# Kernel tuning notes

Hardware: AMD Instinct MI355X
Metric: run time of the kernel (lower is better)

The kernel has to match this reference:

```python
import jax, jax.numpy as jnp
import numpy as np

MAX_NORM = 1.0 - 1e-5  # Poincare ball (c=1) boundary clip, geoopt-style
NUM_HEADS = 8

def _norm(x):
    return jnp.sqrt(jnp.sum(x * x, axis=-1, keepdims=True) + 1e-30)

def projx(x):
    n = _norm(x)
    return jnp.where(n > MAX_NORM, x * (MAX_NORM / n), x)

def expmap0(u):
    n = _norm(u)
    return jnp.tanh(n) * u / n

def logmap0(x):
    n = _norm(x)
    return jnp.arctanh(jnp.minimum(n, MAX_NORM)) * x / n

def mobius_add(x, y):
    xy = jnp.sum(x * y, axis=-1, keepdims=True)
    x2 = jnp.sum(x * x, axis=-1, keepdims=True)
    y2 = jnp.sum(y * y, axis=-1, keepdims=True)
    num = (1.0 + 2.0 * xy + y2) * x + (1.0 - x2) * y
    den = 1.0 + 2.0 * xy + x2 * y2
    return num / jnp.maximum(den, 1e-15)

def mobius_matvec(M, x):
    xn = _norm(x)
    mx = x @ M.T
    mxn = _norm(mx)
    return jnp.tanh(mxn / xn * jnp.arctanh(jnp.minimum(xn, MAX_NORM))) * mx / mxn

def man_linear(x, W, b):
    # Manifold_Linear: mobius matvec + mobius bias add + project (geoopt MobiusLinear)
    return projx(mobius_add(mobius_matvec(W, x), b))

def mob_relu(x):
    # Mob_Act(ReLU): act in tangent space at origin
    return projx(expmap0(jax.nn.relu(logmap0(x))))

def layer_norm(x, g, b):
    mu = jnp.mean(x, axis=-1, keepdims=True)
    v = jnp.var(x, axis=-1, keepdims=True)
    return (x - mu) / jnp.sqrt(v + 1e-5) * g + b

def mha_tan_space(x_q, x_kv, Wq, bq, Wk, bk, Wv, bv, Wo, bo, num_heads):
    # ManifoldMHA with att_metric='tan_space': manifold linear projections,
    # scaled dot-product attention in the tangent space at the origin.
    q = logmap0(man_linear(x_q, Wq, bq))   # (S, B, E)
    k = logmap0(man_linear(x_kv, Wk, bk))  # (T, B, E)
    v = logmap0(man_linear(x_kv, Wv, bv))  # (T, B, E)
    S, B, E = q.shape
    hd = E // num_heads
    def split(t):  # (T,B,E) -> (B,H,T,hd)
        return t.reshape(t.shape[0], B, num_heads, hd).transpose(1, 2, 0, 3)
    qh, kh, vh = split(q), split(k), split(v)
    scores = jnp.einsum('bhqd,bhkd->bhqk', qh, kh) / np.sqrt(hd).astype(np.float32)
    attn = jax.nn.softmax(scores, axis=-1)
    o = jnp.einsum('bhqk,bhkd->bhqd', attn, vh)  # (B,H,S,hd)
    o = o.transpose(2, 0, 1, 3).reshape(S, B, E)
    o = expmap0(o)
    return man_linear(o, Wo, bo)

def forward_block(x, ln1_g, ln1_b, ln2_g, ln2_b, Wq, bq, Wk, bk, Wv, bv, Wo, bo, W1, b1, W2, b2):
    residual = x
    h = expmap0(layer_norm(logmap0(x), ln1_g, ln1_b))
    h = mha_tan_space(h, h, Wq, bq, Wk, bk, Wv, bv, Wo, bo, NUM_HEADS)
    h = projx(h)
    h = projx(mobius_add(h, residual))
    residual = h
    h = projx(expmap0(layer_norm(logmap0(h), ln2_g, ln2_b)))
    h = mob_relu(man_linear(h, W1, b1))   # fc1 = Manifold_Linear + Mob_Act
    h = projx(h)                          # act_dropout (identity, eval) + projx
    h = mob_relu(man_linear(h, W2, b2))   # fc2
    h = projx(mobius_add(h, residual))
    return h

def setup_inputs() -> dict:
    key = jax.random.key(0)
    ks = jax.random.split(key, 18)
    S, B, E, F = 128, 256, 512, 2048
    sE = 1.0 / np.sqrt(E)
    sF = 1.0 / np.sqrt(F)
    # input points must lie inside the unit ball: randn scaled small
    x = jax.random.normal(ks[0], (S, B, E), jnp.float32) * 0.02
    def w(k, o, i, s):
        return jax.random.normal(k, (o, i), jnp.float32) * s
    def bias(k, d):
        return jax.random.normal(k, (d,), jnp.float32) * 1e-3
    return {
        'x': x,
        'ln1_g': jnp.ones((E,), jnp.float32), 'ln1_b': jnp.zeros((E,), jnp.float32),
        'ln2_g': jnp.ones((E,), jnp.float32), 'ln2_b': jnp.zeros((E,), jnp.float32),
        'Wq': w(ks[1], E, E, sE), 'bq': bias(ks[2], E),
        'Wk': w(ks[3], E, E, sE), 'bk': bias(ks[4], E),
        'Wv': w(ks[5], E, E, sE), 'bv': bias(ks[6], E),
        'Wo': w(ks[7], E, E, sE), 'bo': bias(ks[8], E),
        'W1': w(ks[9], F, E, sE), 'b1': bias(ks[10], F),
        'W2': w(ks[11], E, F, sF), 'b2': bias(ks[12], E),
    }

def reference(x, ln1_g, ln1_b, ln2_g, ln2_b, Wq, bq, Wk, bk, Wv, bv, Wo, bo, W1, b1, W2, b2):
    return forward_block(x, ln1_g, ln1_b, ln2_g, ln2_b, Wq, bq, Wk, bk, Wv, bv, Wo, bo, W1, b1, W2, b2)
```

## Files before the change

kernel.cpp:

```cpp
#include <hip/hip_runtime.h>
#include <math.h>

#define S_DIM 128
#define B_DIM 256
#define E_DIM 512
#define F_DIM 2048
#define N_ROWS (S_DIM * B_DIM)
#define CH 8192
#define MAXN 0.99999f

typedef __bf16 bf16x8 __attribute__((ext_vector_type(8)));
typedef float f32x4 __attribute__((ext_vector_type(4)));

__device__ __forceinline__ float frcp(float x) { return __builtin_amdgcn_rcpf(x); }
__device__ __forceinline__ float frsq(float x) { return __builtin_amdgcn_rsqf(x); }
__device__ __forceinline__ float fexp2(float x) { return __builtin_amdgcn_exp2f(x); }
__device__ __forceinline__ float flog2(float x) { return __builtin_amdgcn_logf(x); }
__device__ __forceinline__ float fatanh(float x) {
  return 0.34657359f * flog2((1.f + x) * frcp(1.f - x));
}
__device__ __forceinline__ float ftanh(float x) {
  float t = fexp2(x * -2.88539008f);
  return (1.f - t) * frcp(1.f + t);
}

__device__ __forceinline__ ushort f2bf(float f) {
  __bf16 h = (__bf16)f;
  return __builtin_bit_cast(ushort, h);
}
__device__ __forceinline__ uint pack2(float a, float b) {
  return (uint)f2bf(a) | ((uint)f2bf(b) << 16);
}
__device__ __forceinline__ void ldbf8(const ushort* p, float (&f)[8]) {
  uint4 u = *reinterpret_cast<const uint4*>(p);
  f[0] = __uint_as_float(u.x << 16);
  f[1] = __uint_as_float(u.x & 0xFFFF0000u);
  f[2] = __uint_as_float(u.y << 16);
  f[3] = __uint_as_float(u.y & 0xFFFF0000u);
  f[4] = __uint_as_float(u.z << 16);
  f[5] = __uint_as_float(u.z & 0xFFFF0000u);
  f[6] = __uint_as_float(u.w << 16);
  f[7] = __uint_as_float(u.w & 0xFFFF0000u);
}

__device__ __forceinline__ void gld16(const ushort* g, ushort* l) {
  __builtin_amdgcn_global_load_lds(
      (const __attribute__((address_space(1))) void*)g,
      (__attribute__((address_space(3))) void*)l, 16, 0, 0);
}

template <int K>
__device__ __forceinline__ void waveRed(float (&v)[K]) {
#pragma unroll
  for (int o = 1; o < 64; o <<= 1) {
#pragma unroll
    for (int i = 0; i < K; ++i) v[i] += __shfl_xor(v[i], o);
  }
}

__global__ __launch_bounds__(256) void k_f2bf(const float* __restrict__ in,
                                              ushort* __restrict__ out, int n) {
  for (int i = blockIdx.x * 256 + threadIdx.x; i < n; i += gridDim.x * 256)
    out[i] = f2bf(in[i]);
}

__global__ void k_bsums(const float* __restrict__ bq, const float* __restrict__ bk,
                        const float* __restrict__ bv, const float* __restrict__ g1,
                        const float* __restrict__ lb1, float* __restrict__ bs) {
  int lane = threadIdx.x;
  float p[6];
#pragma unroll
  for (int i = 0; i < 6; ++i) p[i] = 0.f;
  for (int i = lane; i < E_DIM; i += 64) {
    float a = bq[i]; p[0] += a * a;
    a = bk[i]; p[1] += a * a;
    a = bv[i]; p[2] += a * a;
    float g = g1[i], l = lb1[i];
    p[3] += g * g; p[4] += g * l; p[5] += l * l;
  }
  waveRed<6>(p);
  if (lane == 0) {
    bs[0] = p[0]; bs[1] = p[1]; bs[2] = p[2];
    bs[7] = p[3]; bs[8] = p[4]; bs[9] = p[5];
  }
}

__global__ __launch_bounds__(256) void k_stage1(
    const float* __restrict__ x, const float* __restrict__ g,
    const float* __restrict__ bb, const float* __restrict__ bs,
    ushort* __restrict__ h, float* __restrict__ hn) {
  int wv = threadIdx.x >> 6, lane = threadIdx.x & 63;
  int row = blockIdx.x * 8 + wv * 2;
  size_t base = (size_t)row * E_DIM + lane * 8;
  float v[2][8], gv[8], bv[8];
  *(float4*)&v[0][0] = *(const float4*)(x + base);
  *(float4*)&v[0][4] = *(const float4*)(x + base + 4);
  *(float4*)&v[1][0] = *(const float4*)(x + base + E_DIM);
  *(float4*)&v[1][4] = *(const float4*)(x + base + E_DIM + 4);
  *(float4*)&gv[0] = *(const float4*)(g + lane * 8);
  *(float4*)&gv[4] = *(const float4*)(g + lane * 8 + 4);
  *(float4*)&bv[0] = *(const float4*)(bb + lane * 8);
  *(float4*)&bv[4] = *(const float4*)(bb + lane * 8 + 4);
  float s[10];
#pragma unroll
  for (int i = 0; i < 10; ++i) s[i] = 0.f;
#pragma unroll
  for (int i = 0; i < 8; ++i) {
    float gg = gv[i] * gv[i], gb = gv[i] * bv[i];
#pragma unroll
    for (int r2 = 0; r2 < 2; ++r2) {
      float vv = v[r2][i];
      s[r2 * 5 + 0] += vv * vv;
      s[r2 * 5 + 1] += vv;
      s[r2 * 5 + 2] += vv * vv * gg;
      s[r2 * 5 + 3] += vv * gg;
      s[r2 * 5 + 4] += vv * gb;
    }
  }
  waveRed<10>(s);
  float Sg2 = bs[7], Sgb = bs[8], Sb2 = bs[9];
#pragma unroll
  for (int r2 = 0; r2 < 2; ++r2) {
    float T0 = s[r2 * 5 + 0], T1 = s[r2 * 5 + 1], T2 = s[r2 * 5 + 2];
    float T3 = s[r2 * 5 + 3], T4 = s[r2 * 5 + 4];
    float se = T0 + 1e-30f;
    float rn = frsq(se);
    float n = se * rn;
    float a = fatanh(fminf(n, MAXN)) * rn;
    float mu = a * T1 * (1.f / 512.f);
    float var = fmaxf(a * a * T0 * (1.f / 512.f) - mu * mu, 0.f);
    float rstd = frsq(var + 1e-5f);
    float A = a * rstd, B = -mu * rstd;
    float se2 = fmaxf(A * A * T2 + 2.f * A * B * T3 + 2.f * A * T4 +
                          B * B * Sg2 + 2.f * B * Sgb + Sb2, 0.f) + 1e-30f;
    float rn2 = frsq(se2);
    float n2 = se2 * rn2;
    float th = ftanh(n2);
    float f = th * rn2;
    float e[8];
#pragma unroll
    for (int i = 0; i < 8; ++i) e[i] = (A * v[r2][i] + B) * gv[i] + bv[i];
    uint4 o = {pack2(e[0] * f, e[1] * f), pack2(e[2] * f, e[3] * f),
               pack2(e[4] * f, e[5] * f), pack2(e[6] * f, e[7] * f)};
    *reinterpret_cast<uint4*>(h + base + r2 * E_DIM) = o;
    if (lane == 0) hn[row + r2] = th;
  }
}

__global__ __launch_bounds__(256) void k_gemm_bf16(
    const ushort* __restrict__ A, const ushort* __restrict__ B,
    float* __restrict__ C, int K, int M, int kseg,
    unsigned long long partStride, int obf, int GX, int GY) {
  __shared__ __align__(16) ushort As[128 * 32];
  __shared__ __align__(16) ushort Bs[128 * 32];
  int b = blockIdx.x;
  int rx = b & 7, kk2 = b >> 3;
  int bx = kk2 % GX;
  int gg = rx + 8 * (kk2 / GX);
  int by = gg % GY, bz = gg / GY;
  int tid = threadIdx.x;
  int w = tid >> 6, lane = tid & 63;
  int wm = w >> 1, wn = w & 1;
  size_t row0 = (size_t)by * 128;
  size_t col0 = (size_t)bx * 128;
  int k0 = bz * kseg;

  const ushort* gA =
      A + (row0 + w * 32 + (lane >> 2)) * (size_t)K + (lane & 3) * 8 + k0;
  const ushort* gB =
      B + (col0 + w * 32 + (lane >> 2)) * (size_t)K + (lane & 3) * 8 + k0;
  ushort* lA = As + (w * 32) * 32;
  ushort* lB = Bs + (w * 32) * 32;
  const int rowK16 = 16 * K;

  int fro = (lane & 15) * 32 + (lane >> 4) * 8;
  const ushort* raA = As + (wm * 64) * 32 + fro;
  const ushort* raB = Bs + (wn * 64) * 32 + fro;

  f32x4 zero = {0.f, 0.f, 0.f, 0.f};
  f32x4 acc[4][4];
#pragma unroll
  for (int i = 0; i < 4; ++i)
#pragma unroll
    for (int j = 0; j < 4; ++j) acc[i][j] = zero;

  for (int kt = 0; kt < kseg; kt += 32) {
    __syncthreads();
    gld16(gA + kt, lA);
    gld16(gA + kt + rowK16, lA + 16 * 32);
    gld16(gB + kt, lB);
    gld16(gB + kt + rowK16, lB + 16 * 32);
    __syncthreads();
    bf16x8 af[4], bfv[4];
#pragma unroll
    for (int t = 0; t < 4; ++t) {
      af[t] = *reinterpret_cast<const bf16x8*>(raA + t * 512);
      bfv[t] = *reinterpret_cast<const bf16x8*>(raB + t * 512);
    }
#pragma unroll
    for (int i = 0; i < 4; ++i)
#pragma unroll
      for (int j = 0; j < 4; ++j)
        acc[i][j] = __builtin_amdgcn_mfma_f32_16x16x32_bf16(af[i], bfv[j],
                                                            acc[i][j], 0, 0, 0);
  }
  int crow = wm * 64 + (lane >> 4) * 4;
  int ccol = (int)col0 + wn * 64 + (lane & 15);
  if (obf) {
    ushort* Cu = (ushort*)C;
#pragma unroll
    for (int ti = 0; ti < 4; ++ti) {
      size_t r = row0 + crow + ti * 16;
#pragma unroll
      for (int tj = 0; tj < 4; ++tj) {
        int cc = ccol + tj * 16;
#pragma unroll
        for (int reg = 0; reg < 4; ++reg)
          Cu[(r + reg) * (size_t)M + cc] = f2bf(acc[ti][tj][reg]);
      }
    }
  } else {
    float* Cz = C + (size_t)bz * partStride;
#pragma unroll
    for (int ti = 0; ti < 4; ++ti) {
      size_t r = row0 + crow + ti * 16;
#pragma unroll
      for (int tj = 0; tj < 4; ++tj) {
        int cc = ccol + tj * 16;
#pragma unroll
        for (int reg = 0; reg < 4; ++reg)
          Cz[(r + reg) * (size_t)M + cc] = acc[ti][tj][reg];
      }
    }
  }
}

__global__ __launch_bounds__(256) void k_epi_qkv(const ushort* __restrict__ mx,
                                                 const float* __restrict__ xn_arr,
                                                 const float* __restrict__ bias,
                                                 const float* __restrict__ bs_sb2,
                                                 ushort* __restrict__ qout) {
  int wv = threadIdx.x >> 6, lane = threadIdx.x & 63;
  int row = blockIdx.x * 8 + wv * 2;
  size_t base = (size_t)row * E_DIM + lane * 8;
  float m[2][8], bv[8];
  ldbf8(mx + base, m[0]);
  ldbf8(mx + base + E_DIM, m[1]);
  *(float4*)&bv[0] = *(const float4*)(bias + lane * 8);
  *(float4*)&bv[4] = *(const float4*)(bias + lane * 8 + 4);
  float s[4];
#pragma unroll
  for (int i = 0; i < 4; ++i) s[i] = 0.f;
#pragma unroll
  for (int i = 0; i < 8; ++i) {
#pragma unroll
    for (int r2 = 0; r2 < 2; ++r2) {
      s[r2 * 2 + 0] += m[r2][i] * m[r2][i];
      s[r2 * 2 + 1] += m[r2][i] * bv[i];
    }
  }
  waveRed<4>(s);
  float S2 = *bs_sb2;
#pragma unroll
  for (int r2 = 0; r2 < 2; ++r2) {
    float S0 = s[r2 * 2 + 0], S1 = s[r2 * 2 + 1];
    float se = S0 + 1e-30f;
    float rmx = frsq(se);
    float mxn = se * rmx;
    float xn = xn_arr[row + r2];
    float aa = fatanh(fminf(xn, MAXN));
    float tt = ftanh(mxn * frcp(xn) * aa);
    float c = tt * rmx;
    float xy = c * S1, y2 = S2, x2 = tt * tt;
    float c1 = 1.f + 2.f * xy + y2, c2 = 1.f - x2;
    float iden = frcp(fmaxf(1.f + 2.f * xy + x2 * y2, 1e-15f));
    float cc1 = c1 * c * iden, cc2 = c2 * iden;
    float un2 = fmaxf(cc1 * cc1 * S0 + 2.f * cc1 * cc2 * S1 + cc2 * cc2 * S2, 0.f);
    float ue = un2 + 1e-30f;
    float run = frsq(ue);
    float un = ue * run;
    float ne = fminf(un, MAXN);
    float f = fatanh(ne) * run;
    float u[8];
#pragma unroll
    for (int i = 0; i < 8; ++i) u[i] = (cc1 * m[r2][i] + cc2 * bv[i]) * f;
    uint4 o = {pack2(u[0], u[1]), pack2(u[2], u[3]), pack2(u[4], u[5]),
               pack2(u[6], u[7])};
    *reinterpret_cast<uint4*>(qout + base + r2 * E_DIM) = o;
  }
}

__global__ __launch_bounds__(256) void k_attn(const ushort* __restrict__ q,
                                              const ushort* __restrict__ k,
                                              const ushort* __restrict__ v,
                                              ushort* __restrict__ o) {
  __shared__ __align__(16) ushort smem[27136];
  ushort* Qs = smem;
  ushort* Ks = smem + 9216;
  ushort* VTs = smem + 18432;
  ushort* Ps = smem;
  int bh = blockIdx.x;
  int b = bh >> 3, h = bh & 7;
  int tid = threadIdx.x;
  int w = tid >> 6, lane = tid & 63;
  const size_t BE = (size_t)B_DIM * E_DIM;
  size_t gbase = (size_t)b * E_DIM + (size_t)h * 64;

  {
    int s = tid >> 1, half = (tid & 1) * 32;
    const ushort* qr = q + gbase + (size_t)s * BE + half;
    const ushort* kr = k + gbase + (size_t)s * BE + half;
    const ushort* vr = v + gbase + (size_t)s * BE + half;
#pragma unroll
    for (int j = 0; j < 4; ++j) {
      *reinterpret_cast<uint4*>(&Qs[s * 72 + half + j * 8]) =
          *reinterpret_cast<const uint4*>(qr + j * 8);
      *reinterpret_cast<uint4*>(&Ks[s * 72 + half + j * 8]) =
          *reinterpret_cast<const uint4*>(kr + j * 8);
    }
    ushort tv[32];
#pragma unroll
    for (int j = 0; j < 4; ++j)
      *reinterpret_cast<uint4*>(&tv[j * 8]) =
          *reinterpret_cast<const uint4*>(vr + j * 8);
#pragma unroll
    for (int d = 0; d < 32; ++d) VTs[(half + d) * 136 + s] = tv[d];
  }
  __syncthreads();

  f32x4 zero = {0.f, 0.f, 0.f, 0.f};
  f32x4 sacc[2][8];
#pragma unroll
  for (int i = 0; i < 2; ++i)
#pragma unroll
    for (int j = 0; j < 8; ++j) sacc[i][j] = zero;
  {
    const ushort* qb = Qs + (w * 32 + (lane & 15)) * 72 + (lane >> 4) * 8;
    const ushort* kb = Ks + (lane & 15) * 72 + (lane >> 4) * 8;
#pragma unroll
    for (int kk = 0; kk < 2; ++kk) {
      bf16x8 a0 = *reinterpret_cast<const bf16x8*>(qb + kk * 32);
      bf16x8 a1 = *reinterpret_cast<const bf16x8*>(qb + 16 * 72 + kk * 32);
#pragma unroll
      for (int tj = 0; tj < 8; ++tj) {
        bf16x8 bf = *reinterpret_cast<const bf16x8*>(kb + tj * 16 * 72 + kk * 32);
        sacc[0][tj] = __builtin_amdgcn_mfma_f32_16x16x32_bf16(a0, bf,
                                                              sacc[0][tj], 0, 0, 0);
        sacc[1][tj] = __builtin_amdgcn_mfma_f32_16x16x32_bf16(a1, bf,
                                                              sacc[1][tj], 0, 0, 0);
      }
    }
  }

#pragma unroll
  for (int ti = 0; ti < 2; ++ti) {
#pragma unroll
    for (int r = 0; r < 4; ++r) {
      float mx = -1e30f;
#pragma unroll
      for (int tj = 0; tj < 8; ++tj) mx = fmaxf(mx, sacc[ti][tj][r]);
      mx = fmaxf(mx, __shfl_xor(mx, 1));
      mx = fmaxf(mx, __shfl_xor(mx, 2));
      mx = fmaxf(mx, __shfl_xor(mx, 4));
      mx = fmaxf(mx, __shfl_xor(mx, 8));
      float l = 0.f;
#pragma unroll
      for (int tj = 0; tj < 8; ++tj) {
        float e = fexp2((sacc[ti][tj][r] - mx) * (0.125f * 1.44269504f));
        sacc[ti][tj][r] = e;
        l += e;
      }
      l += __shfl_xor(l, 1);
      l += __shfl_xor(l, 2);
      l += __shfl_xor(l, 4);
      l += __shfl_xor(l, 8);
      float inv = frcp(l);
#pragma unroll
      for (int tj = 0; tj < 8; ++tj) sacc[ti][tj][r] *= inv;
    }
  }

  __syncthreads();
  {
    int qr0 = w * 32 + (lane >> 4) * 4;
    int kc = lane & 15;
#pragma unroll
    for (int ti = 0; ti < 2; ++ti)
#pragma unroll
      for (int tj = 0; tj < 8; ++tj)
#pragma unroll
        for (int r = 0; r < 4; ++r)
          Ps[(qr0 + ti * 16 + r) * 136 + tj * 16 + kc] =
              f2bf(sacc[ti][tj][r]);
  }
  __syncthreads();

  f32x4 oacc[2][4];
#pragma unroll
  for (int i = 0; i < 2; ++i)
#pragma unroll
    for (int j = 0; j < 4; ++j) oacc[i][j] = zero;
  {
    const ushort* pb = Ps + (w * 32 + (lane & 15)) * 136 + (lane >> 4) * 8;
    const ushort* vb = VTs + (lane & 15) * 136 + (lane >> 4) * 8;
#pragma unroll
    for (int kk = 0; kk < 4; ++kk) {
      bf16x8 a0 = *reinterpret_cast<const bf16x8*>(pb + kk * 32);
      bf16x8 a1 = *reinterpret_cast<const bf16x8*>(pb + 16 * 136 + kk * 32);
#pragma unroll
      for (int tj = 0; tj < 4; ++tj) {
        bf16x8 bv = *reinterpret_cast<const bf16x8*>(vb + tj * 16 * 136 + kk * 32);
        oacc[0][tj] = __builtin_amdgcn_mfma_f32_16x16x32_bf16(a0, bv,
                                                              oacc[0][tj], 0, 0, 0);
        oacc[1][tj] = __builtin_amdgcn_mfma_f32_16x16x32_bf16(a1, bv,
                                                              oacc[1][tj], 0, 0, 0);
      }
    }
  }

  {
    int qr0 = w * 32 + (lane >> 4) * 4;
    int dc = lane & 15;
#pragma unroll
    for (int ti = 0; ti < 2; ++ti)
#pragma unroll
      for (int tj = 0; tj < 4; ++tj)
#pragma unroll
        for (int r = 0; r < 4; ++r)
          o[(size_t)(qr0 + ti * 16 + r) * BE + gbase + tj * 16 + dc] =
              f2bf(oacc[ti][tj][r]);
  }
}

__global__ __launch_bounds__(256) void k_expmap_rows(const ushort* __restrict__ in,
                                                     ushort* __restrict__ out,
                                                     float* __restrict__ nrm) {
  int wv = threadIdx.x >> 6, lane = threadIdx.x & 63;
  int row = blockIdx.x * 8 + wv * 2;
  size_t base = (size_t)row * E_DIM + lane * 8;
  float v[2][8];
  ldbf8(in + base, v[0]);
  ldbf8(in + base + E_DIM, v[1]);
  float s[2] = {0.f, 0.f};
#pragma unroll
  for (int i = 0; i < 8; ++i) {
    s[0] += v[0][i] * v[0][i];
    s[1] += v[1][i] * v[1][i];
  }
  waveRed<2>(s);
#pragma unroll
  for (int r2 = 0; r2 < 2; ++r2) {
    float se = s[r2] + 1e-30f;
    float rn = frsq(se);
    float n = se * rn;
    float th = ftanh(n);
    float f = th * rn;
    uint4 o = {pack2(v[r2][0] * f, v[r2][1] * f), pack2(v[r2][2] * f, v[r2][3] * f),
               pack2(v[r2][4] * f, v[r2][5] * f), pack2(v[r2][6] * f, v[r2][7] * f)};
    *reinterpret_cast<uint4*>(out + base + r2 * E_DIM) = o;
    if (lane == 0) nrm[row + r2] = th;
  }
}

__global__ __launch_bounds__(256) void k_epi_attnout(
    const ushort* __restrict__ mo, const float* __restrict__ xn_arr,
    const float* __restrict__ bo, const float* __restrict__ xin,
    const float* __restrict__ g2, const float* __restrict__ b2,
    ushort* __restrict__ h2, float* __restrict__ h2n,
    ushort* __restrict__ r2o) {
  int row = blockIdx.x * 4 + (threadIdx.x >> 6);
  int lane = threadIdx.x & 63;
  size_t base = (size_t)row * E_DIM + lane * 8;
  float m[8], bv[8];
  ldbf8(mo + base, m);
  *(float4*)&bv[0] = *(const float4*)(bo + lane * 8);
  *(float4*)&bv[4] = *(const float4*)(bo + lane * 8 + 4);
  float s[5] = {0.f, 0.f, 0.f, 0.f, 0.f};
#pragma unroll
  for (int i = 0; i < 8; ++i) {
    s[0] += m[i] * m[i]; s[1] += m[i] * bv[i]; s[2] += bv[i] * bv[i];
    s[3] += m[i]; s[4] += bv[i];
  }
  waveRed<5>(s);
  float se = s[0] + 1e-30f;
  float rmx = frsq(se);
  float mxn = se * rmx;
  float xn = xn_arr[row];
  float aa = fatanh(fminf(xn, MAXN));
  float tt = ftanh(mxn * frcp(xn) * aa);
  float c = tt * rmx;
  float xy = c * s[1], y2 = s[2], x2 = tt * tt;
  float c1 = 1.f + 2.f * xy + y2, c2 = 1.f - x2;
  float iden = frcp(fmaxf(1.f + 2.f * xy + x2 * y2, 1e-15f));
  float cc1 = c1 * c * iden, cc2 = c2 * iden;
  float un2 = fmaxf(cc1 * cc1 * s[0] + 2.f * cc1 * cc2 * s[1] + cc2 * cc2 * s[2], 0.f);
  float ue = un2 + 1e-30f;
  float run = frsq(ue);
  float un = ue * run;
  float ps = un > MAXN ? MAXN * run : 1.f;
  float zn = fminf(un, MAXN);
  float z[8];
#pragma unroll
  for (int i = 0; i < 8; ++i) z[i] = (cc1 * m[i] + cc2 * bv[i]) * ps;
  float sumz = ps * (cc1 * s[3] + cc2 * s[4]);
  float r[8];
  *(float4*)&r[0] = *(const float4*)(xin + base);
  *(float4*)&r[4] = *(const float4*)(xin + base + 4);
  float t2[3] = {0.f, 0.f, 0.f};
#pragma unroll
  for (int i = 0; i < 8; ++i) {
    t2[0] += z[i] * r[i]; t2[1] += r[i] * r[i]; t2[2] += r[i];
  }
  waveRed<3>(t2);
  float xy2 = t2[0], y22 = t2[1], x22 = zn * zn;
  float d1 = 1.f + 2.f * xy2 + y22, d2 = 1.f - x22;
  float iden2 = frcp(fmaxf(1.f + 2.f * xy2 + x22 * y22, 1e-15f));
  float wn2 = fmaxf(iden2 * iden2 *
                        (d1 * d1 * x22 + 2.f * d1 * d2 * xy2 + d2 * d2 * y22),
                    0.f);
  float we = wn2 + 1e-30f;
  float rwn = frsq(we);
  float wn = we * rwn;
  float ps2 = wn > MAXN ? MAXN * rwn : 1.f;
  float w[8];
#pragma unroll
  for (int i = 0; i < 8; ++i) w[i] = (d1 * z[i] + d2 * r[i]) * iden2 * ps2;
  uint4 ro = {pack2(w[0], w[1]), pack2(w[2], w[3]), pack2(w[4], w[5]),
              pack2(w[6], w[7])};
  *reinterpret_cast<uint4*>(r2o + base) = ro;
  float ne = fminf(wn, MAXN);
  float ath = fatanh(ne);
  float lf = ath * frcp(ne);
  float sumw = ps2 * iden2 * (d1 * sumz + d2 * t2[2]);
  float mu = lf * sumw * (1.f / 512.f);
  float var = fmaxf(ath * ath * (1.f / 512.f) - mu * mu, 0.f);
  float rstd = frsq(var + 1e-5f);
  float gv[8], b2v[8];
  *(float4*)&gv[0] = *(const float4*)(g2 + lane * 8);
  *(float4*)&gv[4] = *(const float4*)(g2 + lane * 8 + 4);
  *(float4*)&b2v[0] = *(const float4*)(b2 + lane * 8);
  *(float4*)&b2v[4] = *(const float4*)(b2 + lane * 8 + 4);
  float e[8];
  float s3[1] = {0.f};
#pragma unroll
  for (int i = 0; i < 8; ++i) {
    e[i] = (lf * w[i] - mu) * rstd * gv[i] + b2v[i];
    s3[0] += e[i] * e[i];
  }
  waveRed<1>(s3);
  float s3e = s3[0] + 1e-30f;
  float rn3 = frsq(s3e);
  float n3 = s3e * rn3;
  float en = ftanh(n3);
  float f = en * rn3;
  if (en > MAXN) f *= MAXN * frcp(en);
  uint4 o = {pack2(e[0] * f, e[1] * f), pack2(e[2] * f, e[3] * f),
             pack2(e[4] * f, e[5] * f), pack2(e[6] * f, e[7] * f)};
  *reinterpret_cast<uint4*>(h2 + base) = o;
  if (lane == 0) h2n[row] = fminf(en, MAXN);
}

__global__ __launch_bounds__(256) void k_epi_ffn1(const ushort* __restrict__ mr_,
                                                  const float* __restrict__ xn_arr,
                                                  const float* __restrict__ bias,
                                                  ushort* __restrict__ hid,
                                                  float* __restrict__ hn_out) {
  int wv = threadIdx.x >> 6, lane = threadIdx.x & 63;
  int row = blockIdx.x * 8 + wv * 2;
  const ushort* mr = mr_ + (size_t)row * F_DIM + lane * 32;
  const float* br = bias + lane * 32;
  float m[2][32], bv[32];
#pragma unroll
  for (int j = 0; j < 4; ++j) {
    ldbf8(mr + j * 8, *(float(*)[8])&m[0][j * 8]);
    ldbf8(mr + F_DIM + j * 8, *(float(*)[8])&m[1][j * 8]);
  }
#pragma unroll
  for (int j = 0; j < 8; ++j)
    *(float4*)&bv[j * 4] = *(const float4*)(br + j * 4);
  float s[5];
#pragma unroll
  for (int i = 0; i < 5; ++i) s[i] = 0.f;
#pragma unroll
  for (int i = 0; i < 32; ++i) {
#pragma unroll
    for (int r2 = 0; r2 < 2; ++r2) {
      s[r2 * 2 + 0] += m[r2][i] * m[r2][i];
      s[r2 * 2 + 1] += m[r2][i] * bv[i];
    }
    s[4] += bv[i] * bv[i];
  }
  waveRed<5>(s);
  float s2[2] = {0.f, 0.f};
#pragma unroll
  for (int r2 = 0; r2 < 2; ++r2) {
    float S0 = s[r2 * 2 + 0], S1 = s[r2 * 2 + 1], S2 = s[4];
    float se = S0 + 1e-30f;
    float rmx = frsq(se);
    float mxn = se * rmx;
    float xn = xn_arr[row + r2];
    float aa = fatanh(fminf(xn, MAXN));
    float tt = ftanh(mxn * frcp(xn) * aa);
    float c = tt * rmx;
    float xy = c * S1, y2 = S2, x2 = tt * tt;
    float c1 = 1.f + 2.f * xy + y2, c2 = 1.f - x2;
    float iden = frcp(fmaxf(1.f + 2.f * xy + x2 * y2, 1e-15f));
    float cc1 = c1 * c * iden, cc2 = c2 * iden;
    float un2 = fmaxf(cc1 * cc1 * S0 + 2.f * cc1 * cc2 * S1 + cc2 * cc2 * S2, 0.f);
    float ue = un2 + 1e-30f;
    float run = frsq(ue);
    float un = ue * run;
    float zn = fminf(un, MAXN);
    float lf = fatanh(zn) * run;
#pragma unroll
    for (int i = 0; i < 32; ++i) {
      m[r2][i] = fmaxf((cc1 * m[r2][i] + cc2 * bv[i]) * lf, 0.f);
      s2[r2] += m[r2][i] * m[r2][i];
    }
  }
  waveRed<2>(s2);
#pragma unroll
  for (int r2 = 0; r2 < 2; ++r2) {
    float s2e = s2[r2] + 1e-30f;
    float rrn = frsq(s2e);
    float rn = s2e * rrn;
    float en = ftanh(rn);
    float f = en * rrn;
    if (en > MAXN) f *= MAXN * frcp(en);
    ushort* hr = hid + (size_t)(row + r2) * F_DIM + lane * 32;
#pragma unroll
    for (int j = 0; j < 4; ++j) {
      uint4 o = {pack2(m[r2][j * 8 + 0] * f, m[r2][j * 8 + 1] * f),
                 pack2(m[r2][j * 8 + 2] * f, m[r2][j * 8 + 3] * f),
                 pack2(m[r2][j * 8 + 4] * f, m[r2][j * 8 + 5] * f),
                 pack2(m[r2][j * 8 + 6] * f, m[r2][j * 8 + 7] * f)};
      *reinterpret_cast<uint4*>(hr + j * 8) = o;
    }
    if (lane == 0) hn_out[row + r2] = fminf(en, MAXN);
  }
}

__global__ __launch_bounds__(256) void k_epi_final(
    const float* __restrict__ m2, const float* __restrict__ xn_arr,
    const float* __restrict__ bias, const ushort* __restrict__ res,
    float* __restrict__ out) {
  int wv = threadIdx.x >> 6, lane = threadIdx.x & 63;
  int row = blockIdx.x * 8 + wv * 2;
  size_t base = (size_t)row * E_DIM + lane * 8;
  const size_t P2 = (size_t)CH * E_DIM;
  float m[2][8], bv[8], q[2][8];
#pragma unroll
  for (int r2 = 0; r2 < 2; ++r2) {
    float ta[8], tb[8];
    *(float4*)&ta[0] = *(const float4*)(m2 + base + r2 * E_DIM);
    *(float4*)&ta[4] = *(const float4*)(m2 + base + r2 * E_DIM + 4);
    *(float4*)&tb[0] = *(const float4*)(m2 + P2 + base + r2 * E_DIM);
    *(float4*)&tb[4] = *(const float4*)(m2 + P2 + base + r2 * E_DIM + 4);
#pragma unroll
    for (int i = 0; i < 8; ++i) m[r2][i] = ta[i] + tb[i];
    ldbf8(res + base + r2 * E_DIM, q[r2]);
  }
  *(float4*)&bv[0] = *(const float4*)(bias + lane * 8);
  *(float4*)&bv[4] = *(const float4*)(bias + lane * 8 + 4);
  float s[7];
#pragma unroll
  for (int i = 0; i < 7; ++i) s[i] = 0.f;
#pragma unroll
  for (int i = 0; i < 8; ++i) {
#pragma unroll
    for (int r2 = 0; r2 < 2; ++r2) {
      s[r2 * 3 + 0] += m[r2][i] * m[r2][i];
      s[r2 * 3 + 1] += m[r2][i] * bv[i];
      s[r2 * 3 + 2] += q[r2][i] * q[r2][i];
    }
    s[6] += bv[i] * bv[i];
  }
  waveRed<7>(s);
  float r[2][8];
  float s2[4];
#pragma unroll
  for (int i = 0; i < 4; ++i) s2[i] = 0.f;
#pragma unroll
  for (int r2 = 0; r2 < 2; ++r2) {
    float S0 = s[r2 * 3 + 0], S1 = s[r2 * 3 + 1], S2 = s[6];
    float se = S0 + 1e-30f;
    float rmx = frsq(se);
    float mxn = se * rmx;
    float xn = xn_arr[row + r2];
    float aa = fatanh(fminf(xn, MAXN));
    float tt = ftanh(mxn * frcp(xn) * aa);
    float c = tt * rmx;
    float xy = c * S1, y2 = S2, x2 = tt * tt;
    float c1 = 1.f + 2.f * xy + y2, c2 = 1.f - x2;
    float iden = frcp(fmaxf(1.f + 2.f * xy + x2 * y2, 1e-15f));
    float cc1 = c1 * c * iden, cc2 = c2 * iden;
    float un2 = fmaxf(cc1 * cc1 * S0 + 2.f * cc1 * cc2 * S1 + cc2 * cc2 * S2, 0.f);
    float ue = un2 + 1e-30f;
    float run = frsq(ue);
    float un = ue * run;
    float zn = fminf(un, MAXN);
    float lf = fatanh(zn) * run;
#pragma unroll
    for (int i = 0; i < 8; ++i) {
      r[r2][i] = fmaxf((cc1 * m[r2][i] + cc2 * bv[i]) * lf, 0.f);
      s2[r2 * 2 + 0] += r[r2][i] * r[r2][i];
      s2[r2 * 2 + 1] += r[r2][i] * q[r2][i];
    }
  }
  waveRed<4>(s2);
#pragma unroll
  for (int r2 = 0; r2 < 2; ++r2) {
    float s2e = s2[r2 * 2 + 0] + 1e-30f;
    float rrn = frsq(s2e);
    float rn = s2e * rrn;
    float en = ftanh(rn);
    float f = en * rrn;
    if (en > MAXN) f *= MAXN * frcp(en);
    float hn = fminf(en, MAXN);
    float xy2 = f * s2[r2 * 2 + 1], y22 = s[r2 * 3 + 2], x22 = hn * hn;
    float d1 = 1.f + 2.f * xy2 + y22, d2 = 1.f - x22;
    float iden2 = frcp(fmaxf(1.f + 2.f * xy2 + x22 * y22, 1e-15f));
    float wn2 = fmaxf(iden2 * iden2 *
                          (d1 * d1 * x22 + 2.f * d1 * d2 * xy2 + d2 * d2 * y22),
                      0.f);
    float we = wn2 + 1e-30f;
    float rwn = frsq(we);
    float wn = we * rwn;
    float ps2 = wn > MAXN ? MAXN * rwn : 1.f;
    float w[8];
#pragma unroll
    for (int i = 0; i < 8; ++i)
      w[i] = (d1 * r[r2][i] * f + d2 * q[r2][i]) * iden2 * ps2;
    *(float4*)(out + base + r2 * E_DIM) = *(float4*)&w[0];
    *(float4*)(out + base + r2 * E_DIM + 4) = *(float4*)&w[4];
  }
}

extern "C" void kernel_launch(void* const* d_in, const int* in_sizes, int n_in,
                              void* d_out, int out_size, void* d_ws,
                              size_t ws_size, hipStream_t stream) {
  const float* x   = (const float*)d_in[0];
  const float* g1  = (const float*)d_in[1];
  const float* lb1 = (const float*)d_in[2];
  const float* g2  = (const float*)d_in[3];
  const float* lb2 = (const float*)d_in[4];
  const float* Wq  = (const float*)d_in[5];
  const float* bq  = (const float*)d_in[6];
  const float* Wk  = (const float*)d_in[7];
  const float* bk  = (const float*)d_in[8];
  const float* Wv  = (const float*)d_in[9];
  const float* bv  = (const float*)d_in[10];
  const float* Wo  = (const float*)d_in[11];
  const float* bo  = (const float*)d_in[12];
  const float* W1  = (const float*)d_in[13];
  const float* b1  = (const float*)d_in[14];
  const float* W2  = (const float*)d_in[15];
  const float* b2  = (const float*)d_in[16];
  float* out = (float*)d_out;
  float* ws = (float*)d_ws;

  const size_t NE = (size_t)N_ROWS * E_DIM;
  const size_t WF = (4 * (size_t)E_DIM * E_DIM +
                     2 * (size_t)F_DIM * E_DIM) / 2;
  ushort* Cb   = (ushort*)ws;
  ushort* r2u  = (ushort*)(ws + NE / 2);
  float* R_a = ws + NE;
  float* R_q = ws + NE + NE / 2;
  float* R_k = ws + 2 * NE;
  float* R_v = ws + 2 * NE + NE / 2;
  ushort* wqb = (ushort*)(ws + 3 * NE);
  ushort* wkb = wqb + (size_t)E_DIM * E_DIM;
  ushort* wvb = wkb + (size_t)E_DIM * E_DIM;
  ushort* wob = wvb + (size_t)E_DIM * E_DIM;
  ushort* w1b = wob + (size_t)E_DIM * E_DIM;
  ushort* w2b = w1b + (size_t)F_DIM * E_DIM;
  float* n_h1 = ws + 3 * NE + WF;
  float* n_oe = n_h1 + N_ROWS;
  float* n_h2 = n_oe + N_ROWS;
  float* n_h3 = n_h2 + N_ROWS;
  float* bs = n_h3 + N_ROWS;
  const size_t need = (3 * NE + WF + 4 * (size_t)N_ROWS + 16) * sizeof(float);
  if (ws_size < need) return;

  k_bsums<<<1, 64, 0, stream>>>(bq, bk, bv, g1, lb1, bs);
  k_f2bf<<<256, 256, 0, stream>>>(Wq, wqb, E_DIM * E_DIM);
  k_f2bf<<<256, 256, 0, stream>>>(Wk, wkb, E_DIM * E_DIM);
  k_f2bf<<<256, 256, 0, stream>>>(Wv, wvb, E_DIM * E_DIM);
  k_f2bf<<<256, 256, 0, stream>>>(Wo, wob, E_DIM * E_DIM);
  k_f2bf<<<512, 256, 0, stream>>>(W1, w1b, F_DIM * E_DIM);
  k_f2bf<<<512, 256, 0, stream>>>(W2, w2b, F_DIM * E_DIM);

  ushort* h1b = (ushort*)R_a;
  ushort* qb = (ushort*)R_q;
  ushort* kb = (ushort*)R_k;
  ushort* vb = (ushort*)R_v;

  k_stage1<<<N_ROWS / 8, 256, 0, stream>>>(x, g1, lb1, bs, h1b, n_h1);
  const int gE = 4 * 256;
  k_gemm_bf16<<<gE, 256, 0, stream>>>(h1b, wqb, (float*)Cb, E_DIM, E_DIM,
                                      E_DIM, 0, 1, 4, 256);
  k_epi_qkv<<<N_ROWS / 8, 256, 0, stream>>>(Cb, n_h1, bq, bs + 0, qb);
  k_gemm_bf16<<<gE, 256, 0, stream>>>(h1b, wkb, (float*)Cb, E_DIM, E_DIM,
                                      E_DIM, 0, 1, 4, 256);
  k_epi_qkv<<<N_ROWS / 8, 256, 0, stream>>>(Cb, n_h1, bk, bs + 1, kb);
  k_gemm_bf16<<<gE, 256, 0, stream>>>(h1b, wvb, (float*)Cb, E_DIM, E_DIM,
                                      E_DIM, 0, 1, 4, 256);
  k_epi_qkv<<<N_ROWS / 8, 256, 0, stream>>>(Cb, n_h1, bv, bs + 2, vb);

  k_attn<<<B_DIM * 8, 256, 0, stream>>>(qb, kb, vb, Cb);
  ushort* oeb = (ushort*)R_a;
  k_expmap_rows<<<N_ROWS / 8, 256, 0, stream>>>(Cb, oeb, n_oe);

  ushort* h2b = (ushort*)R_a;
  k_gemm_bf16<<<gE, 256, 0, stream>>>(oeb, wob, (float*)Cb, E_DIM, E_DIM,
                                      E_DIM, 0, 1, 4, 256);
  k_epi_attnout<<<N_ROWS / 4, 256, 0, stream>>>(Cb, n_oe, bo, x, g2, lb2,
                                                h2b, n_h2, r2u);

  ushort* m1 = Cb;
  ushort* hidb = (ushort*)R_v;
  float* m2 = R_q;
  for (int c = 0; c < N_ROWS / CH; ++c) {
    size_t ro = (size_t)c * CH;
    k_gemm_bf16<<<16 * 64, 256, 0, stream>>>(
        h2b + ro * E_DIM, w1b, (float*)m1, E_DIM, F_DIM, E_DIM, 0, 1, 16, 64);
    k_epi_ffn1<<<CH / 8, 256, 0, stream>>>(m1, n_h2 + ro, b1, hidb, n_h3 + ro);
    k_gemm_bf16<<<4 * 64 * 2, 256, 0, stream>>>(
        hidb, w2b, m2, F_DIM, E_DIM, F_DIM / 2,
        (unsigned long long)((size_t)CH * E_DIM), 0, 4, 64);
    k_epi_final<<<CH / 8, 256, 0, stream>>>(m2, n_h3 + ro, b2,
                                            r2u + ro * E_DIM, out + ro * E_DIM);
  }
}
```

Measured before the change: 820.8 us.

## Double-buffer LDS tiles in bf16 GEMM to overlap global loads with MFMA

The GEMM kernel now keeps two LDS buffers for the A and B tiles. It prefetches the next K-slice into the alternate buffer while MFMAs run on the current one, replacing the two syncthreads per iteration with a single waitcnt plus barrier. The goal is to hide global-to-LDS load latency behind compute. In exchange it doubles LDS use to 32KB per block, which may reduce occupancy.

```diff
diff --git a/kernel.cpp b/kernel.cpp
--- a/kernel.cpp
+++ b/kernel.cpp
@@ -151,8 +151,8 @@
     const ushort* __restrict__ A, const ushort* __restrict__ B,
     float* __restrict__ C, int K, int M, int kseg,
     unsigned long long partStride, int obf, int GX, int GY) {
-  __shared__ __align__(16) ushort As[128 * 32];
-  __shared__ __align__(16) ushort Bs[128 * 32];
+  __shared__ __align__(16) ushort As[2][128 * 32];
+  __shared__ __align__(16) ushort Bs[2][128 * 32];
   int b = blockIdx.x;
   int rx = b & 7, kk2 = b >> 3;
   int bx = kk2 % GX;
@@ -169,13 +169,9 @@
       A + (row0 + w * 32 + (lane >> 2)) * (size_t)K + (lane & 3) * 8 + k0;
   const ushort* gB =
       B + (col0 + w * 32 + (lane >> 2)) * (size_t)K + (lane & 3) * 8 + k0;
-  ushort* lA = As + (w * 32) * 32;
-  ushort* lB = Bs + (w * 32) * 32;
+  const int lofs = (w * 32) * 32;
   const int rowK16 = 16 * K;
-
   int fro = (lane & 15) * 32 + (lane >> 4) * 8;
-  const ushort* raA = As + (wm * 64) * 32 + fro;
-  const ushort* raB = Bs + (wn * 64) * 32 + fro;
 
   f32x4 zero = {0.f, 0.f, 0.f, 0.f};
   f32x4 acc[4][4];
@@ -184,13 +180,25 @@
 #pragma unroll
     for (int j = 0; j < 4; ++j) acc[i][j] = zero;
 
+  gld16(gA, As[0] + lofs);
+  gld16(gA + rowK16, As[0] + lofs + 16 * 32);
+  gld16(gB, Bs[0] + lofs);
+  gld16(gB + rowK16, Bs[0] + lofs + 16 * 32);
+  asm volatile("s_waitcnt vmcnt(0)" ::: "memory");
+  __builtin_amdgcn_s_barrier();
+  __builtin_amdgcn_sched_barrier(0);
+
+  int cur = 0;
   for (int kt = 0; kt < kseg; kt += 32) {
-    __syncthreads();
-    gld16(gA + kt, lA);
-    gld16(gA + kt + rowK16, lA + 16 * 32);
-    gld16(gB + kt, lB);
-    gld16(gB + kt + rowK16, lB + 16 * 32);
-    __syncthreads();
+    if (kt + 32 < kseg) {
+      int nxt = cur ^ 1;
+      gld16(gA + kt + 32, As[nxt] + lofs);
+      gld16(gA + kt + 32 + rowK16, As[nxt] + lofs + 16 * 32);
+      gld16(gB + kt + 32, Bs[nxt] + lofs);
+      gld16(gB + kt + 32 + rowK16, Bs[nxt] + lofs + 16 * 32);
+    }
+    const ushort* raA = As[cur] + (wm * 64) * 32 + fro;
+    const ushort* raB = Bs[cur] + (wn * 64) * 32 + fro;
     bf16x8 af[4], bfv[4];
 #pragma unroll
     for (int t = 0; t < 4; ++t) {
@@ -203,7 +211,12 @@
       for (int j = 0; j < 4; ++j)
         acc[i][j] = __builtin_amdgcn_mfma_f32_16x16x32_bf16(af[i], bfv[j],
                                                             acc[i][j], 0, 0, 0);
-  }
+    asm volatile("s_waitcnt vmcnt(0)" ::: "memory");
+    __builtin_amdgcn_s_barrier();
+    __builtin_amdgcn_sched_barrier(0);
+    cur ^= 1;
+  }
+
   int crow = wm * 64 + (lane >> 4) * 4;
   int ccol = (int)col0 + wn * 64 + (lane & 15);
   if (obf) {
```

Measured after the change: 762.9 us. 1.08x faster.
